# Optimization experiments

Measured on AMD Instinct MI355X. Metric: run time of the kernel, lower is better.

The kernel has to match this reference:

```python
import jax, jax.numpy as jnp
import numpy as np

BATCH = 4096
NUM_INPUTS = 784
WIDTH = 16000        # neurons per logic layer, divisible by NUM_CLASSES
N_HIDDEN = 4         # width->width layers stacked for scan (plus the input layer)
NUM_CLASSES = 10


def setup_inputs() -> dict:
    key = jax.random.key(0)
    ks = jax.random.split(key, 7)
    x = jax.random.bernoulli(ks[0], 0.5, (BATCH, NUM_INPUTS))
    idx_a0 = jax.random.randint(ks[1], (WIDTH,), 0, NUM_INPUTS, dtype=jnp.int32)
    idx_b0 = jax.random.randint(ks[2], (WIDTH,), 0, NUM_INPUTS, dtype=jnp.int32)
    neg0 = jax.random.bernoulli(ks[3], 0.5, (WIDTH, 2))
    idx_a = jax.random.randint(ks[4], (N_HIDDEN, WIDTH), 0, WIDTH, dtype=jnp.int32)
    idx_b = jax.random.randint(ks[5], (N_HIDDEN, WIDTH), 0, WIDTH, dtype=jnp.int32)
    neg = jax.random.bernoulli(ks[6], 0.5, (N_HIDDEN, WIDTH, 2))
    return {"x": x, "idx_a0": idx_a0, "idx_b0": idx_b0, "neg0": neg0,
            "idx_a": idx_a, "idx_b": idx_b, "neg": neg}


def _gate(a, b, nf):
    # gate = (maybe-NOT a) AND (maybe-NOT b); NOT on booleans == XOR with flag
    return (a ^ nf[:, 0]) & (b ^ nf[:, 1])


def reference(x, idx_a0, idx_b0, neg0, idx_a, idx_b, neg):
    # input layer: gather wires from the boolean input
    h = _gate(x[:, idx_a0], x[:, idx_b0], neg0)  # [BATCH, WIDTH] bool

    def step(h, p):
        ia, ib, nf = p
        return _gate(h[:, ia], h[:, ib], nf), None

    h, _ = jax.lax.scan(step, h, (idx_a, idx_b, neg))
    # GroupSum: popcount per class group -> int32 logits
    out = h.reshape(BATCH, NUM_CLASSES, WIDTH // NUM_CLASSES).sum(-1, dtype=jnp.int32)
    return out
```

## Files before the change

### kernel.cpp

```cpp
#include <hip/hip_runtime.h>


#define NIN   784
#define WIDTH 16000
#define SW    16384
#define NH    4
#define NC    10
#define GPC   1600
#define NBLK  128
#define TPB   1024

typedef unsigned int u32;

__global__ void desc_kernel(const int* __restrict__ ia0, const int* __restrict__ ib0,
                            const int* __restrict__ n0,
                            const int* __restrict__ ia, const int* __restrict__ ib,
                            const int* __restrict__ n, u32* __restrict__ desc) {
    int t = blockIdx.x * blockDim.x + threadIdx.x;
    if (t >= (NH + 1) * SW) return;
    int l = t >> 14;
    int g = t & (SW - 1);
    u32 d = 0;
    if (g < WIDTH) {
        int a, b, na, nb;
        if (l == 0) { a = ia0[g]; b = ib0[g]; na = n0[2 * g]; nb = n0[2 * g + 1]; }
        else {
            int o = (l - 1) * WIDTH + g;
            a = ia[o]; b = ib[o]; na = n[2 * o]; nb = n[2 * o + 1];
        }
        d = (u32)a | ((u32)b << 14) | (na ? (1u << 28) : 0u) | (nb ? (1u << 29) : 0u);
    }
    desc[t] = d;
}

__launch_bounds__(TPB, 4)
__global__ void net_kernel(const int* __restrict__ x, const u32* __restrict__ desc,
                           int* __restrict__ out) {
    __shared__ __align__(16) u32 xw[NIN];
    __shared__ __align__(16) u32 bufA[SW];
    __shared__ __align__(16) u32 bufB[SW];

    int w = blockIdx.x;
    int t = threadIdx.x;

    uint4 dreg[4];
    {
        const uint4* d0 = (const uint4*)desc;
#pragma unroll
        for (int j = 0; j < 4; ++j) dreg[j] = d0[t + j * TPB];
    }

    if (t < NIN) {
        const int* base = x + (size_t)(w * 32) * NIN + t;
        u32 acc = 0;
#pragma unroll
        for (int r = 0; r < 32; ++r)
            acc |= (base[(size_t)r * NIN] != 0 ? 1u : 0u) << r;
        xw[t] = acc;
    }
    __syncthreads();

    u32* cur = xw;
#pragma unroll
    for (int l = 0; l <= NH; ++l) {
        u32* dst = (l & 1) ? bufB : bufA;

        u32 av[12], bv[12];

#define ISSUE(S, SLOT) { \
        u32 d0 = dreg[S].x, d1 = dreg[S].y, d2 = dreg[S].z, d3 = dreg[S].w; \
        av[4*(SLOT)+0] = cur[d0 & 0x3FFFu]; bv[4*(SLOT)+0] = cur[(d0 >> 14) & 0x3FFFu]; \
        av[4*(SLOT)+1] = cur[d1 & 0x3FFFu]; bv[4*(SLOT)+1] = cur[(d1 >> 14) & 0x3FFFu]; \
        av[4*(SLOT)+2] = cur[d2 & 0x3FFFu]; bv[4*(SLOT)+2] = cur[(d2 >> 14) & 0x3FFFu]; \
        av[4*(SLOT)+3] = cur[d3 & 0x3FFFu]; bv[4*(SLOT)+3] = cur[(d3 >> 14) & 0x3FFFu]; }

#define CONSUME(S, SLOT) { \
        u32 d0 = dreg[S].x, d1 = dreg[S].y, d2 = dreg[S].z, d3 = dreg[S].w; \
        uint4 r; \
        r.x = (av[4*(SLOT)+0] ^ (0u - ((d0 >> 28) & 1u))) & (bv[4*(SLOT)+0] ^ (0u - ((d0 >> 29) & 1u))); \
        r.y = (av[4*(SLOT)+1] ^ (0u - ((d1 >> 28) & 1u))) & (bv[4*(SLOT)+1] ^ (0u - ((d1 >> 29) & 1u))); \
        r.z = (av[4*(SLOT)+2] ^ (0u - ((d2 >> 28) & 1u))) & (bv[4*(SLOT)+2] ^ (0u - ((d2 >> 29) & 1u))); \
        r.w = (av[4*(SLOT)+3] ^ (0u - ((d3 >> 28) & 1u))) & (bv[4*(SLOT)+3] ^ (0u - ((d3 >> 29) & 1u))); \
        *(uint4*)(dst + 4 * (t + (S) * TPB)) = r; }

        ISSUE(0, 0);
        ISSUE(1, 1);
        ISSUE(2, 2);
        CONSUME(0, 0);
        ISSUE(3, 0);
        CONSUME(1, 1);
        CONSUME(2, 2);
        CONSUME(3, 0);

#undef ISSUE
#undef CONSUME

        if (l < NH) {
            const uint4* dq = (const uint4*)(desc + (size_t)(l + 1) * SW);
#pragma unroll
            for (int j = 0; j < 4; ++j) dreg[j] = dq[t + j * TPB];
        }
        __syncthreads();
        cur = dst;
    }
    u32* res = bufA;

    int wave = t >> 6, lane = t & 63;
    if (wave < NC) {
        int c = wave;
        const u32* base = res + c * GPC;
        u32 p0 = 0, p1 = 0, p2 = 0, p3 = 0, p4 = 0;
#define CSA5(VAL) { u32 cy = (VAL); u32 s; \
        s = p0; p0 = s ^ cy; cy = s & cy; \
        s = p1; p1 = s ^ cy; cy = s & cy; \
        s = p2; p2 = s ^ cy; cy = s & cy; \
        s = p3; p3 = s ^ cy; cy = s & cy; \
        s = p4; p4 = s ^ cy; }
#pragma unroll
        for (int k = 0; k < 6; ++k) {
            uint4 v = *(const uint4*)(base + 4 * lane + 256 * k);
            CSA5(v.x); CSA5(v.y); CSA5(v.z); CSA5(v.w);
        }
        CSA5(base[1536 + lane]);
#undef CSA5

        u32 pl[11];
        pl[0] = p0; pl[1] = p1; pl[2] = p2; pl[3] = p3; pl[4] = p4;
#pragma unroll
        for (int s = 0; s < 6; ++s) {
            int np = 5 + s;
            u32 q[11];
#pragma unroll
            for (int i = 0; i < 11; ++i) if (i < np) q[i] = __shfl_xor(pl[i], 1 << s, 64);
            u32 carry = 0;
#pragma unroll
            for (int i = 0; i < 11; ++i) if (i < np) {
                u32 a = pl[i], b = q[i];
                u32 xr = a ^ b;
                pl[i] = xr ^ carry;
                carry = (a & b) | (carry & xr);
            }
            pl[np] = carry;
        }

        if (lane < 32) {
            int cntv = 0;
#pragma unroll
            for (int i = 0; i < 11; ++i) cntv += (int)((pl[i] >> lane) & 1u) << i;
            out[((size_t)w * 32 + lane) * NC + c] = cntv;
        }
    }
}

extern "C" void kernel_launch(void* const* d_in, const int* in_sizes, int n_in,
                              void* d_out, int out_size, void* d_ws, size_t ws_size,
                              hipStream_t stream) {
    const int* x      = (const int*)d_in[0];
    const int* idx_a0 = (const int*)d_in[1];
    const int* idx_b0 = (const int*)d_in[2];
    const int* neg0   = (const int*)d_in[3];
    const int* idx_a  = (const int*)d_in[4];
    const int* idx_b  = (const int*)d_in[5];
    const int* neg    = (const int*)d_in[6];
    int* out = (int*)d_out;

    u32* desc = (u32*)d_ws;

    int ndesc = (NH + 1) * SW;
    desc_kernel<<<(ndesc + 255) / 256, 256, 0, stream>>>(
        idx_a0, idx_b0, neg0, idx_a, idx_b, neg, desc);

    net_kernel<<<NBLK, TPB, 0, stream>>>(x, desc, out);
}
```

Baseline: 86.64 us.

## Drop descriptor-packing kernel and read raw index/negation arrays in main kernel

Removes the separate desc_kernel launch that packed indices and negation flags into 32-bit descriptors, and has net_kernel load idx_a, idx_b and neg directly from global memory each layer, interleaved with the shared-memory gathers. This saves a kernel launch and the workspace write/read round trip. In exchange each of the 128 blocks reads about four times more index data (three int arrays instead of one packed word), and the slot-3 index is clamped to 3999 so those threads repeat valid loads while the widths stay aligned with the original layout.

```diff
diff --git a/kernel.cpp b/kernel.cpp
--- a/kernel.cpp
+++ b/kernel.cpp
@@ -12,29 +12,12 @@
 
 typedef unsigned int u32;
 
-__global__ void desc_kernel(const int* __restrict__ ia0, const int* __restrict__ ib0,
-                            const int* __restrict__ n0,
-                            const int* __restrict__ ia, const int* __restrict__ ib,
-                            const int* __restrict__ n, u32* __restrict__ desc) {
-    int t = blockIdx.x * blockDim.x + threadIdx.x;
-    if (t >= (NH + 1) * SW) return;
-    int l = t >> 14;
-    int g = t & (SW - 1);
-    u32 d = 0;
-    if (g < WIDTH) {
-        int a, b, na, nb;
-        if (l == 0) { a = ia0[g]; b = ib0[g]; na = n0[2 * g]; nb = n0[2 * g + 1]; }
-        else {
-            int o = (l - 1) * WIDTH + g;
-            a = ia[o]; b = ib[o]; na = n[2 * o]; nb = n[2 * o + 1];
-        }
-        d = (u32)a | ((u32)b << 14) | (na ? (1u << 28) : 0u) | (nb ? (1u << 29) : 0u);
-    }
-    desc[t] = d;
-}
-
 __launch_bounds__(TPB, 4)
-__global__ void net_kernel(const int* __restrict__ x, const u32* __restrict__ desc,
+__global__ void net_kernel(const int* __restrict__ x,
+                           const int* __restrict__ ia0, const int* __restrict__ ib0,
+                           const int* __restrict__ n0,
+                           const int* __restrict__ iah, const int* __restrict__ ibh,
+                           const int* __restrict__ nh,
                            int* __restrict__ out) {
     __shared__ __align__(16) u32 xw[NIN];
     __shared__ __align__(16) u32 bufA[SW];
@@ -42,13 +25,6 @@
 
     int w = blockIdx.x;
     int t = threadIdx.x;
-
-    uint4 dreg[4];
-    {
-        const uint4* d0 = (const uint4*)desc;
-#pragma unroll
-        for (int j = 0; j < 4; ++j) dreg[j] = d0[t + j * TPB];
-    }
 
     if (t < NIN) {
         const int* base = x + (size_t)(w * 32) * NIN + t;
@@ -60,46 +36,61 @@
     }
     __syncthreads();
 
+    int i3 = t + 3 * TPB; if (i3 > 3999) i3 = 3999;
+
     u32* cur = xw;
 #pragma unroll
     for (int l = 0; l <= NH; ++l) {
         u32* dst = (l & 1) ? bufB : bufA;
+        const int* pa = l ? iah + (size_t)(l - 1) * WIDTH : ia0;
+        const int* pb = l ? ibh + (size_t)(l - 1) * WIDTH : ib0;
+        const int* pn = l ? nh  + (size_t)(l - 1) * 2 * WIDTH : n0;
 
+        uint4 ta[2], tb[2];
+        uint4 rn0[3], rn1[3];
         u32 av[12], bv[12];
 
-#define ISSUE(S, SLOT) { \
-        u32 d0 = dreg[S].x, d1 = dreg[S].y, d2 = dreg[S].z, d3 = dreg[S].w; \
-        av[4*(SLOT)+0] = cur[d0 & 0x3FFFu]; bv[4*(SLOT)+0] = cur[(d0 >> 14) & 0x3FFFu]; \
-        av[4*(SLOT)+1] = cur[d1 & 0x3FFFu]; bv[4*(SLOT)+1] = cur[(d1 >> 14) & 0x3FFFu]; \
-        av[4*(SLOT)+2] = cur[d2 & 0x3FFFu]; bv[4*(SLOT)+2] = cur[(d2 >> 14) & 0x3FFFu]; \
-        av[4*(SLOT)+3] = cur[d3 & 0x3FFFu]; bv[4*(SLOT)+3] = cur[(d3 >> 14) & 0x3FFFu]; }
+#define IDX(S) ((S) == 3 ? i3 : (t + (S) * TPB))
+
+#define LOADRAW(S, B, SLOT) { \
+        int ii = IDX(S); \
+        ta[B]  = *(const uint4*)(pa + 4 * ii); \
+        tb[B]  = *(const uint4*)(pb + 4 * ii); \
+        rn0[SLOT] = *(const uint4*)(pn + 8 * ii); \
+        rn1[SLOT] = *(const uint4*)(pn + 8 * ii + 4); }
+
+#define ISSUE(B, SLOT) { \
+        av[4*(SLOT)+0] = cur[(u32)ta[B].x]; bv[4*(SLOT)+0] = cur[(u32)tb[B].x]; \
+        av[4*(SLOT)+1] = cur[(u32)ta[B].y]; bv[4*(SLOT)+1] = cur[(u32)tb[B].y]; \
+        av[4*(SLOT)+2] = cur[(u32)ta[B].z]; bv[4*(SLOT)+2] = cur[(u32)tb[B].z]; \
+        av[4*(SLOT)+3] = cur[(u32)ta[B].w]; bv[4*(SLOT)+3] = cur[(u32)tb[B].w]; }
 
 #define CONSUME(S, SLOT) { \
-        u32 d0 = dreg[S].x, d1 = dreg[S].y, d2 = dreg[S].z, d3 = dreg[S].w; \
         uint4 r; \
-        r.x = (av[4*(SLOT)+0] ^ (0u - ((d0 >> 28) & 1u))) & (bv[4*(SLOT)+0] ^ (0u - ((d0 >> 29) & 1u))); \
-        r.y = (av[4*(SLOT)+1] ^ (0u - ((d1 >> 28) & 1u))) & (bv[4*(SLOT)+1] ^ (0u - ((d1 >> 29) & 1u))); \
-        r.z = (av[4*(SLOT)+2] ^ (0u - ((d2 >> 28) & 1u))) & (bv[4*(SLOT)+2] ^ (0u - ((d2 >> 29) & 1u))); \
-        r.w = (av[4*(SLOT)+3] ^ (0u - ((d3 >> 28) & 1u))) & (bv[4*(SLOT)+3] ^ (0u - ((d3 >> 29) & 1u))); \
+        r.x = (av[4*(SLOT)+0] ^ (0u - (u32)(rn0[SLOT].x != 0))) & (bv[4*(SLOT)+0] ^ (0u - (u32)(rn0[SLOT].y != 0))); \
+        r.y = (av[4*(SLOT)+1] ^ (0u - (u32)(rn0[SLOT].z != 0))) & (bv[4*(SLOT)+1] ^ (0u - (u32)(rn0[SLOT].w != 0))); \
+        r.z = (av[4*(SLOT)+2] ^ (0u - (u32)(rn1[SLOT].x != 0))) & (bv[4*(SLOT)+2] ^ (0u - (u32)(rn1[SLOT].y != 0))); \
+        r.w = (av[4*(SLOT)+3] ^ (0u - (u32)(rn1[SLOT].z != 0))) & (bv[4*(SLOT)+3] ^ (0u - (u32)(rn1[SLOT].w != 0))); \
         *(uint4*)(dst + 4 * (t + (S) * TPB)) = r; }
 
+        LOADRAW(0, 0, 0);
+        LOADRAW(1, 1, 1);
         ISSUE(0, 0);
+        LOADRAW(2, 0, 2);
         ISSUE(1, 1);
-        ISSUE(2, 2);
         CONSUME(0, 0);
-        ISSUE(3, 0);
+        LOADRAW(3, 1, 0);
+        ISSUE(0, 2);
         CONSUME(1, 1);
+        ISSUE(1, 0);
         CONSUME(2, 2);
         CONSUME(3, 0);
 
+#undef LOADRAW
 #undef ISSUE
 #undef CONSUME
+#undef IDX
 
-        if (l < NH) {
-            const uint4* dq = (const uint4*)(desc + (size_t)(l + 1) * SW);
-#pragma unroll
-            for (int j = 0; j < 4; ++j) dreg[j] = dq[t + j * TPB];
-        }
         __syncthreads();
         cur = dst;
     }
@@ -164,11 +155,8 @@
     const int* neg    = (const int*)d_in[6];
     int* out = (int*)d_out;
 
-    u32* desc = (u32*)d_ws;
+    (void)d_ws; (void)ws_size;
 
-    int ndesc = (NH + 1) * SW;
-    desc_kernel<<<(ndesc + 255) / 256, 256, 0, stream>>>(
-        idx_a0, idx_b0, neg0, idx_a, idx_b, neg, desc);
-
-    net_kernel<<<NBLK, TPB, 0, stream>>>(x, desc, out);
+    net_kernel<<<NBLK, TPB, 0, stream>>>(
+        x, idx_a0, idx_b0, neg0, idx_a, idx_b, neg, out);
 }
```

New measurement: 86.28 us. Within noise of the previous version (-0.4%).

## Split gate descriptors into index and mask planes with rolling prefetch

Applied to the files above, without the earlier changes.

The packed 30-bit descriptor per gate is replaced by four separate planes: index A, index B, and full-width negation masks for A and B. This removes the shift-and-mask decode in the inner loop. The kernel now streams descriptors in half-layer chunks with a three-slot rotation, so the loads for the next chunk overlap with the shared-memory gathers and gate computation. The cost is four times more descriptor traffic from global/L2 per layer and higher register pressure from the extra uint4 mask registers.

```diff
diff --git a/kernel.cpp b/kernel.cpp
--- a/kernel.cpp
+++ b/kernel.cpp
@@ -9,6 +9,7 @@
 #define GPC   1600
 #define NBLK  128
 #define TPB   1024
+#define DL    (4 * SW)
 
 typedef unsigned int u32;
 
@@ -20,7 +21,7 @@
     if (t >= (NH + 1) * SW) return;
     int l = t >> 14;
     int g = t & (SW - 1);
-    u32 d = 0;
+    u32 va = 0, vb = 0, ma = 0, mb = 0;
     if (g < WIDTH) {
         int a, b, na, nb;
         if (l == 0) { a = ia0[g]; b = ib0[g]; na = n0[2 * g]; nb = n0[2 * g + 1]; }
@@ -28,9 +29,14 @@
             int o = (l - 1) * WIDTH + g;
             a = ia[o]; b = ib[o]; na = n[2 * o]; nb = n[2 * o + 1];
         }
-        d = (u32)a | ((u32)b << 14) | (na ? (1u << 28) : 0u) | (nb ? (1u << 29) : 0u);
+        va = (u32)a; vb = (u32)b;
+        ma = na ? ~0u : 0u; mb = nb ? ~0u : 0u;
     }
-    desc[t] = d;
+    u32* base = desc + (size_t)l * DL;
+    base[g]          = va;
+    base[SW + g]     = vb;
+    base[2 * SW + g] = ma;
+    base[3 * SW + g] = mb;
 }
 
 __launch_bounds__(TPB, 4)
@@ -43,12 +49,33 @@
     int w = blockIdx.x;
     int t = threadIdx.x;
 
-    uint4 dreg[4];
-    {
-        const uint4* d0 = (const uint4*)desc;
-#pragma unroll
-        for (int j = 0; j < 4; ++j) dreg[j] = d0[t + j * TPB];
-    }
+    uint4 ta[2], tb[2];
+    uint4 ma[3], mb[3];
+    u32 av[12], bv[12];
+
+#define LOADRAW(D, II, B, SLOT) { \
+        int ii = (II); \
+        ta[B]    = *(const uint4*)((D) + 4 * ii); \
+        tb[B]    = *(const uint4*)((D) + SW + 4 * ii); \
+        ma[SLOT] = *(const uint4*)((D) + 2 * SW + 4 * ii); \
+        mb[SLOT] = *(const uint4*)((D) + 3 * SW + 4 * ii); }
+
+#define ISSUE(B, SLOT) { \
+        av[4*(SLOT)+0] = cur[ta[B].x]; bv[4*(SLOT)+0] = cur[tb[B].x]; \
+        av[4*(SLOT)+1] = cur[ta[B].y]; bv[4*(SLOT)+1] = cur[tb[B].y]; \
+        av[4*(SLOT)+2] = cur[ta[B].z]; bv[4*(SLOT)+2] = cur[tb[B].z]; \
+        av[4*(SLOT)+3] = cur[ta[B].w]; bv[4*(SLOT)+3] = cur[tb[B].w]; }
+
+#define CONSUME(S, SLOT) { \
+        uint4 r; \
+        r.x = (av[4*(SLOT)+0] ^ ma[SLOT].x) & (bv[4*(SLOT)+0] ^ mb[SLOT].x); \
+        r.y = (av[4*(SLOT)+1] ^ ma[SLOT].y) & (bv[4*(SLOT)+1] ^ mb[SLOT].y); \
+        r.z = (av[4*(SLOT)+2] ^ ma[SLOT].z) & (bv[4*(SLOT)+2] ^ mb[SLOT].z); \
+        r.w = (av[4*(SLOT)+3] ^ ma[SLOT].w) & (bv[4*(SLOT)+3] ^ mb[SLOT].w); \
+        *(uint4*)(dst + 4 * (t + (S) * TPB)) = r; }
+
+    LOADRAW(desc, t,       0, 0);
+    LOADRAW(desc, t + TPB, 1, 1);
 
     if (t < NIN) {
         const int* base = x + (size_t)(w * 32) * NIN + t;
@@ -64,58 +91,43 @@
 #pragma unroll
     for (int l = 0; l <= NH; ++l) {
         u32* dst = (l & 1) ? bufB : bufA;
+        const int sp = l % 3, sq = (l + 1) % 3, sr = (l + 2) % 3;
+        const u32* D  = desc + (size_t)l * DL;
 
-        u32 av[12], bv[12];
-
-#define ISSUE(S, SLOT) { \
-        u32 d0 = dreg[S].x, d1 = dreg[S].y, d2 = dreg[S].z, d3 = dreg[S].w; \
-        av[4*(SLOT)+0] = cur[d0 & 0x3FFFu]; bv[4*(SLOT)+0] = cur[(d0 >> 14) & 0x3FFFu]; \
-        av[4*(SLOT)+1] = cur[d1 & 0x3FFFu]; bv[4*(SLOT)+1] = cur[(d1 >> 14) & 0x3FFFu]; \
-        av[4*(SLOT)+2] = cur[d2 & 0x3FFFu]; bv[4*(SLOT)+2] = cur[(d2 >> 14) & 0x3FFFu]; \
-        av[4*(SLOT)+3] = cur[d3 & 0x3FFFu]; bv[4*(SLOT)+3] = cur[(d3 >> 14) & 0x3FFFu]; }
-
-#define CONSUME(S, SLOT) { \
-        u32 d0 = dreg[S].x, d1 = dreg[S].y, d2 = dreg[S].z, d3 = dreg[S].w; \
-        uint4 r; \
-        r.x = (av[4*(SLOT)+0] ^ (0u - ((d0 >> 28) & 1u))) & (bv[4*(SLOT)+0] ^ (0u - ((d0 >> 29) & 1u))); \
-        r.y = (av[4*(SLOT)+1] ^ (0u - ((d1 >> 28) & 1u))) & (bv[4*(SLOT)+1] ^ (0u - ((d1 >> 29) & 1u))); \
-        r.z = (av[4*(SLOT)+2] ^ (0u - ((d2 >> 28) & 1u))) & (bv[4*(SLOT)+2] ^ (0u - ((d2 >> 29) & 1u))); \
-        r.w = (av[4*(SLOT)+3] ^ (0u - ((d3 >> 28) & 1u))) & (bv[4*(SLOT)+3] ^ (0u - ((d3 >> 29) & 1u))); \
-        *(uint4*)(dst + 4 * (t + (S) * TPB)) = r; }
-
-        ISSUE(0, 0);
-        ISSUE(1, 1);
-        ISSUE(2, 2);
-        CONSUME(0, 0);
-        ISSUE(3, 0);
-        CONSUME(1, 1);
-        CONSUME(2, 2);
-        CONSUME(3, 0);
-
-#undef ISSUE
-#undef CONSUME
-
+        ISSUE(0, sp);
+        LOADRAW(D, t + 2 * TPB, 0, sr);
+        ISSUE(1, sq);
+        CONSUME(0, sp);
+        LOADRAW(D, t + 3 * TPB, 1, sp);
+        ISSUE(0, sr);
+        CONSUME(1, sq);
+        ISSUE(1, sp);
+        CONSUME(2, sr);
         if (l < NH) {
-            const uint4* dq = (const uint4*)(desc + (size_t)(l + 1) * SW);
-#pragma unroll
-            for (int j = 0; j < 4; ++j) dreg[j] = dq[t + j * TPB];
+            const u32* D2 = desc + (size_t)(l + 1) * DL;
+            LOADRAW(D2, t,       0, sq);
+            LOADRAW(D2, t + TPB, 1, sr);
         }
+        CONSUME(3, sp);
         __syncthreads();
         cur = dst;
     }
+#undef LOADRAW
+#undef ISSUE
+#undef CONSUME
     u32* res = bufA;
 
     int wave = t >> 6, lane = t & 63;
     if (wave < NC) {
         int c = wave;
         const u32* base = res + c * GPC;
-        u32 p0 = 0, p1 = 0, p2 = 0, p3 = 0, p4 = 0;
+        u32 p0 = 0, p1 = 0, p2 = 0, p3v = 0, p4 = 0;
 #define CSA5(VAL) { u32 cy = (VAL); u32 s; \
-        s = p0; p0 = s ^ cy; cy = s & cy; \
-        s = p1; p1 = s ^ cy; cy = s & cy; \
-        s = p2; p2 = s ^ cy; cy = s & cy; \
-        s = p3; p3 = s ^ cy; cy = s & cy; \
-        s = p4; p4 = s ^ cy; }
+        s = p0;  p0  = s ^ cy; cy = s & cy; \
+        s = p1;  p1  = s ^ cy; cy = s & cy; \
+        s = p2;  p2  = s ^ cy; cy = s & cy; \
+        s = p3v; p3v = s ^ cy; cy = s & cy; \
+        s = p4;  p4  = s ^ cy; }
 #pragma unroll
         for (int k = 0; k < 6; ++k) {
             uint4 v = *(const uint4*)(base + 4 * lane + 256 * k);
@@ -125,7 +137,7 @@
 #undef CSA5
 
         u32 pl[11];
-        pl[0] = p0; pl[1] = p1; pl[2] = p2; pl[3] = p3; pl[4] = p4;
+        pl[0] = p0; pl[1] = p1; pl[2] = p2; pl[3] = p3v; pl[4] = p4;
 #pragma unroll
         for (int s = 0; s < 6; ++s) {
             int np = 5 + s;
```

New measurement: 87.77 us. Within noise of the previous version (+1.3%).
